# Kernel tuning notes

Measured on AMD Instinct MI355X. Metric: run time of the kernel, lower is better.

Reference implementation:

```python
import jax, jax.numpy as jnp
import numpy as np

N = 32768       # nodes
E = 65536       # directed edges
B = 512         # graphs (N // B = 64 atoms each)
DIM = 64
NUM_FEAT = 14
EDGE_DIM = 4
NET_HID = 128
CONV_STEPS = 12
S2S_STEPS = 3
NSTEM = 1024
NUM_OUT_STEM = 105

leaky = lambda v: jax.nn.leaky_relu(v, 0.01)


def setup_inputs():
    key = jax.random.key(0)
    ks = jax.random.split(key, 30)
    p = lambda i, shape, s=0.1: jax.random.normal(ks[i], shape, jnp.float32) * s
    return {
        'x': jax.random.normal(ks[0], (N, NUM_FEAT), jnp.float32),
        'edge_attr': jax.random.uniform(ks[1], (E, EDGE_DIM), jnp.float32),
        'edge_index': jax.random.randint(ks[2], (2, E), 0, N),
        'batch': jnp.arange(N, dtype=jnp.int32) // (N // B),  # sorted graph ids, all graphs non-empty
        'stem_idx': jax.random.randint(ks[3], (NSTEM,), 0, N),
        'lin0_w': p(4, (DIM, NUM_FEAT)), 'lin0_b': p(5, (DIM,)),
        'net_w1': p(6, (NET_HID, EDGE_DIM)), 'net_b1': p(7, (NET_HID,)),
        'net_w2': p(8, (DIM * DIM, NET_HID), 0.05), 'net_b2': p(9, (DIM * DIM,), 0.05),
        'conv_root': p(10, (DIM, DIM)), 'conv_bias': p(11, (DIM,)),
        'gru_w_ih': p(12, (3 * DIM, DIM)), 'gru_w_hh': p(13, (3 * DIM, DIM)),
        'gru_b_ih': p(14, (3 * DIM,)), 'gru_b_hh': p(15, (3 * DIM,)),
        'lin1_w': p(16, (8 * DIM, DIM)), 'lin1_b': p(17, (8 * DIM,)),
        'lin2_w': p(18, (NUM_OUT_STEM, 8 * DIM)), 'lin2_b': p(19, (NUM_OUT_STEM,)),
        's2s_w_ih': p(20, (4 * DIM, 2 * DIM)), 's2s_w_hh': p(21, (4 * DIM, DIM)),
        's2s_b_ih': p(22, (4 * DIM,)), 's2s_b_hh': p(23, (4 * DIM,)),
        'lin3_w': p(24, (1, 2 * DIM)), 'lin3_b': p(25, (1,)),
    }


def reference(x, edge_attr, edge_index, batch, stem_idx,
              lin0_w, lin0_b, net_w1, net_b1, net_w2, net_b2,
              conv_root, conv_bias, gru_w_ih, gru_w_hh, gru_b_ih, gru_b_hh,
              lin1_w, lin1_b, lin2_w, lin2_b,
              s2s_w_ih, s2s_w_hh, s2s_b_ih, s2s_b_hh, lin3_w, lin3_b):
    src, dst = edge_index[0], edge_index[1]

    out = leaky(x @ lin0_w.T + lin0_b)               # [N, DIM]
    h = out

    # edge-conditioned weights: constant across conv steps (edge_attr fixed), hoist
    W = (leaky(edge_attr @ net_w1.T + net_b1) @ net_w2.T + net_b2).reshape(E, DIM, DIM)

    deg = jax.ops.segment_sum(jnp.ones((E,), jnp.float32), dst, num_segments=N)
    inv_deg = (1.0 / jnp.maximum(deg, 1.0))[:, None]

    def step(carry, _):
        out, h = carry
        # NNConv: gather src feats, per-edge matmul, scatter-mean to dst, plus root term
        msg = jnp.einsum('ei,eio->eo', out[src], W)                           # [E, DIM]
        agg = jax.ops.segment_sum(msg, dst, num_segments=N) * inv_deg        # scatter-mean
        m = leaky(agg + out @ conv_root + conv_bias)
        # GRU cell (torch gate order r, z, n)
        gi = m @ gru_w_ih.T + gru_b_ih
        gh = h @ gru_w_hh.T + gru_b_hh
        ir, iz, i_n = jnp.split(gi, 3, axis=-1)
        hr, hz, hn = jnp.split(gh, 3, axis=-1)
        r = jax.nn.sigmoid(ir + hr)
        z = jax.nn.sigmoid(iz + hz)
        n = jnp.tanh(i_n + r * hn)
        h_new = (1.0 - z) * n + z * h
        return (h_new, h_new), None

    (out, h), _ = jax.lax.scan(step, (out, h), None, length=CONV_STEPS)

    # per-stem head (stem_idx = precomputed flat node indices)
    stem_feat = out[stem_idx]                                                # [NSTEM, DIM]
    per_stem_out = leaky(stem_feat @ lin1_w.T + lin1_b) @ lin2_w.T + lin2_b  # [NSTEM, 105]

    # Set2Set readout (LSTM with torch gate order i, f, g, o)
    q_star = jnp.zeros((B, 2 * DIM), jnp.float32)
    hh = jnp.zeros((B, DIM), jnp.float32)
    cc = jnp.zeros((B, DIM), jnp.float32)
    for _ in range(S2S_STEPS):
        gates = q_star @ s2s_w_ih.T + s2s_b_ih + hh @ s2s_w_hh.T + s2s_b_hh
        gi_, gf_, gg_, go_ = jnp.split(gates, 4, axis=-1)
        cc = jax.nn.sigmoid(gf_) * cc + jax.nn.sigmoid(gi_) * jnp.tanh(gg_)
        hh = jax.nn.sigmoid(go_) * jnp.tanh(cc)
        q = hh                                                               # [B, DIM]
        e = jnp.sum(out * q[batch], axis=-1)                                 # [N]
        emax = jax.ops.segment_max(e, batch, num_segments=B)
        ee = jnp.exp(e - emax[batch])
        a = ee / jax.ops.segment_sum(ee, batch, num_segments=B)[batch]       # segment softmax
        r_read = jax.ops.segment_sum(a[:, None] * out, batch, num_segments=B)
        q_star = jnp.concatenate([q, r_read], axis=-1)

    sout = q_star @ lin3_w.T + lin3_b                                        # [B, 1]
    return sout, per_stem_out


if __name__ == '__main__':
    o = reference(**setup_inputs())
    print(o[0].shape, o[1].shape)
```

## Files before the change

### kernel.cpp

```cpp
#include <hip/hip_runtime.h>
#include <hip/hip_bf16.h>

#define N_NODES   32768
#define N_EDGES   65536
#define NGRAPH    512
#define DIM       64
#define NFEAT     14
#define NHID      128
#define WCOLS     4096
#define NSTEM     1024
#define NOUT      105

typedef __attribute__((ext_vector_type(8))) short short8;
typedef __attribute__((ext_vector_type(4))) float f32x4;

__device__ __forceinline__ float bf2f(unsigned int u16) {
  union { unsigned int i; float f; } c; c.i = u16 << 16; return c.f;
}
__device__ __forceinline__ unsigned short f2bf(float f) {
  union { float f; unsigned int i; } c; c.f = f;
  return (unsigned short)((c.i + 0x7fffu + ((c.i >> 16) & 1u)) >> 16);
}
__device__ __forceinline__ float leaky(float x) { return x > 0.f ? x : 0.01f * x; }
__device__ __forceinline__ float sigm(float x) { return 1.f / (1.f + expf(-x)); }

constexpr size_t ALN(size_t x) { return (x + 255) & ~(size_t)255; }

constexpr size_t OFF_HIDP = 0;
constexpr size_t SZ_HIDP  = (size_t)N_EDGES * NHID * 2;
constexpr size_t OFF_T2T  = ALN(OFF_HIDP + SZ_HIDP);
constexpr size_t SZ_T2T   = (size_t)WCOLS * NHID * 2;
constexpr size_t OFF_B2T  = ALN(OFF_T2T + SZ_T2T);
constexpr size_t SZ_B2T   = (size_t)WCOLS * 4;
constexpr size_t OFF_STATE= ALN(OFF_B2T + SZ_B2T);
constexpr size_t SZ_STATE = (size_t)N_NODES * DIM * 4;
constexpr size_t OFF_AGG  = ALN(OFF_STATE + SZ_STATE);
constexpr size_t SZ_AGG   = SZ_STATE;
constexpr size_t OFF_IDEG = ALN(OFF_AGG + SZ_AGG);
constexpr size_t SZ_IDEG  = (size_t)N_NODES * 4;
constexpr size_t OFF_CNT  = ALN(OFF_IDEG + SZ_IDEG);
constexpr size_t SZ_CNT   = (size_t)N_NODES * 4;
constexpr size_t OFF_RP   = ALN(OFF_CNT + SZ_CNT);
constexpr size_t SZ_RP    = (size_t)(N_NODES + 1) * 4;
constexpr size_t OFF_CUR  = ALN(OFF_RP + SZ_RP);
constexpr size_t SZ_CUR   = (size_t)N_NODES * 4;
constexpr size_t OFF_SRCP = ALN(OFF_CUR + SZ_CUR);
constexpr size_t SZ_SRCP  = (size_t)N_EDGES * 4;
constexpr size_t OFF_DSTP = ALN(OFF_SRCP + SZ_SRCP);
constexpr size_t SZ_DSTP  = (size_t)N_EDGES * 4;
constexpr size_t OFF_EPOS = ALN(OFF_DSTP + SZ_DSTP);
constexpr size_t SZ_EPOS  = (size_t)N_EDGES * 4;
constexpr size_t OFF_BW1  = ALN(OFF_EPOS + SZ_EPOS);
constexpr size_t SZ_BW1   = 256 * 64 * 2;
constexpr size_t OFF_BW2  = ALN(OFF_BW1 + SZ_BW1);
constexpr size_t SZ_BW2   = 192 * 64 * 2;
constexpr size_t OFF_WIH  = ALN(OFF_BW2 + SZ_BW2);
constexpr size_t SZ_WIH   = 128 * 256 * 4;
constexpr size_t OFF_WHH  = ALN(OFF_WIH + SZ_WIH);
constexpr size_t SZ_WHH   = 64 * 256 * 4;
constexpr size_t OFF_SCL  = ALN(OFF_WHH + SZ_WHH);
constexpr size_t SZ_SCL   = (size_t)N_EDGES * 64 * 4;
constexpr size_t OFF_WT   = ALN(OFF_SCL + SZ_SCL);

__global__ void k_deg(const int* __restrict__ dst, int* __restrict__ cnt) {
  int e = blockIdx.x * 256 + threadIdx.x;
  atomicAdd(&cnt[dst[e]], 1);
}
__global__ __launch_bounds__(1024) void k_scan(const int* __restrict__ cnt,
                                               int* __restrict__ rp,
                                               int* __restrict__ cur,
                                               float* __restrict__ ideg) {
  __shared__ int part[1024];
  const int t = threadIdx.x, base = t * 32;
  int s = 0;
  for (int i = 0; i < 32; ++i) s += cnt[base + i];
  part[t] = s;
  __syncthreads();
  for (int off = 1; off < 1024; off <<= 1) {
    int v = (t >= off) ? part[t - off] : 0;
    __syncthreads();
    part[t] += v;
    __syncthreads();
  }
  int run = part[t] - s;
  for (int i = 0; i < 32; ++i) {
    int c = cnt[base + i];
    rp[base + i] = run; cur[base + i] = run;
    ideg[base + i] = 1.0f / fmaxf((float)c, 1.0f);
    run += c;
  }
  if (t == 1023) rp[N_NODES] = run;
}
__global__ void k_permute(const int* __restrict__ src, const int* __restrict__ dst,
                          int* __restrict__ cur, int* __restrict__ src_p,
                          int* __restrict__ dst_p, int* __restrict__ epos) {
  int e = blockIdx.x * 256 + threadIdx.x;
  int d = dst[e];
  int p = atomicAdd(&cur[d], 1);
  src_p[p] = src[e]; dst_p[p] = d; epos[e] = p;
}
__global__ void k_prep_t2(const float* __restrict__ w2, const float* __restrict__ b2,
                          unsigned short* __restrict__ T2t, float* __restrict__ b2t) {
  int gid = blockIdx.x * 256 + threadIdx.x;
  int r = gid >> 7, h = gid & 127;
  int srow = (r & 63) * 64 + (r >> 6);
  T2t[gid] = f2bf(w2[(size_t)srow * 128 + h]);
  if (h == 0) b2t[r] = b2[srow];
}
__global__ void k_prep_gru(const float* __restrict__ root, const float* __restrict__ whh,
                           const float* __restrict__ wih,
                           unsigned short* __restrict__ BW1, unsigned short* __restrict__ BW2) {
  int gid = blockIdx.x * 256 + threadIdx.x;
  if (gid >= 64 * 448) return;
  int i = gid / 448, c = gid % 448;
  if (c < 64)        BW1[c * 64 + i] = f2bf(root[i * 64 + c]);
  else if (c < 256)  BW1[c * 64 + i] = f2bf(whh[(c - 64) * 64 + i]);
  else               BW2[(c - 256) * 64 + i] = f2bf(wih[(c - 256) * 64 + i]);
}
__global__ void k_prep_s2s(const float* __restrict__ wih, const float* __restrict__ whh,
                           float* __restrict__ wihT, float* __restrict__ whhT) {
  int gid = blockIdx.x * 256 + threadIdx.x;
  if (gid < 32768) { int j = gid >> 8, k = gid & 255; wihT[gid] = wih[k * 128 + j]; }
  else { int g2 = gid - 32768; int j = g2 >> 8, k = g2 & 255; whhT[g2] = whh[k * 64 + j]; }
}
__global__ void k_lin0(const float* __restrict__ x, const float* __restrict__ w,
                       const float* __restrict__ b, float* __restrict__ state) {
  int gid = blockIdx.x * 256 + threadIdx.x;
  int n = gid >> 6, o = gid & 63;
  float acc = b[o];
  #pragma unroll
  for (int f = 0; f < NFEAT; ++f) acc += x[(size_t)n * NFEAT + f] * w[o * NFEAT + f];
  state[gid] = leaky(acc);
}
__global__ void k_hidden(const float* __restrict__ ea, const float* __restrict__ w1,
                         const float* __restrict__ b1, const int* __restrict__ epos,
                         unsigned short* __restrict__ hid_p) {
  int gid = blockIdx.x * 256 + threadIdx.x;
  int e = gid >> 7, h = gid & 127;
  float acc = b1[h];
  #pragma unroll
  for (int d = 0; d < 4; ++d) acc += ea[(size_t)e * 4 + d] * w1[h * 4 + d];
  hid_p[(size_t)epos[e] * 128 + h] = f2bf(leaky(acc));
}

#define WG_PAD 136
__global__ __launch_bounds__(256) void k_wgemm(const unsigned short* __restrict__ A,
                                               const unsigned short* __restrict__ Bt,
                                               const float* __restrict__ b2t,
                                               unsigned short* __restrict__ WtP,
                                               unsigned char* __restrict__ W8,
                                               float* __restrict__ SCL,
                                               int peb) {
  __shared__ __align__(16) unsigned short As[64 * WG_PAD];
  __shared__ __align__(16) unsigned short Bs[64 * WG_PAD];
  __shared__ __align__(16) char pk[64][64];
  const int nb = blockIdx.x, mb = blockIdx.y, t = threadIdx.x;
  #pragma unroll
  for (int j = 0; j < 4; ++j) {
    int c = t + 256 * j;
    int row = c >> 4, col8 = (c & 15) * 8;
    *reinterpret_cast<uint4*>(&As[row * WG_PAD + col8]) =
        *reinterpret_cast<const uint4*>(A + (size_t)(mb * 64 + row) * 128 + col8);
    *reinterpret_cast<uint4*>(&Bs[row * WG_PAD + col8]) =
        *reinterpret_cast<const uint4*>(Bt + (size_t)(nb * 64 + row) * 128 + col8);
  }
  __syncthreads();
  const int wv = t >> 6, ln = t & 63, r = ln & 15, g = ln >> 4;
  f32x4 acc[4] = {};
  #pragma unroll
  for (int ks = 0; ks < 4; ++ks) {
    int k0 = ks * 32 + g * 8;
    short8 a = *reinterpret_cast<const short8*>(&As[(wv * 16 + r) * WG_PAD + k0]);
    #pragma unroll
    for (int nt = 0; nt < 4; ++nt) {
      short8 b = *reinterpret_cast<const short8*>(&Bs[(nt * 16 + r) * WG_PAD + k0]);
      acc[nt] = __builtin_amdgcn_mfma_f32_16x16x32_bf16(a, b, acc[nt], 0, 0, 0);
    }
  }
  float bias[4];
  #pragma unroll
  for (int nt = 0; nt < 4; ++nt) bias[nt] = b2t[nb * 64 + nt * 16 + r];

  if (mb * 64 < peb) {
    #pragma unroll
    for (int nt = 0; nt < 4; ++nt) {
      int col = nb * 64 + nt * 16 + r;
      #pragma unroll
      for (int j = 0; j < 4; ++j) {
        int row = mb * 64 + wv * 16 + g * 4 + j;
        WtP[(size_t)row * WCOLS + col] = f2bf(acc[nt][j] + bias[nt]);
      }
    }
  } else {
    #pragma unroll
    for (int j = 0; j < 4; ++j) {
      int e_l = wv * 16 + g * 4 + j;
      float w[4], m = 0.f;
      #pragma unroll
      for (int nt = 0; nt < 4; ++nt) { w[nt] = acc[nt][j] + bias[nt]; m = fmaxf(m, fabsf(w[nt])); }
      m = fmaxf(m, __shfl_xor(m, 1)); m = fmaxf(m, __shfl_xor(m, 2));
      m = fmaxf(m, __shfl_xor(m, 4)); m = fmaxf(m, __shfl_xor(m, 8));
      float inv = m > 0.f ? 127.f / m : 0.f;
      #pragma unroll
      for (int nt = 0; nt < 4; ++nt)
        pk[e_l][nt * 16 + r] = (char)(int)rintf(w[nt] * inv);
      if (r == 0) {
        size_t e8 = (size_t)(mb * 64 - peb) + e_l;
        SCL[e8 * 64 + nb] = m * (1.f / 127.f);
      }
    }
    __syncthreads();
    int e_l = t >> 2, q4 = t & 3;
    size_t e8 = (size_t)(mb * 64 - peb) + e_l;
    *reinterpret_cast<uint4*>(W8 + e8 * 4096 + nb * 64 + q4 * 16) =
        *reinterpret_cast<const uint4*>(&pk[e_l][q4 * 16]);
  }
}

__global__ __launch_bounds__(256) void k_msg_csr(const unsigned short* __restrict__ WtP,
                                                 const unsigned char* __restrict__ W8,
                                                 const float* __restrict__ SCL,
                                                 int peb, int lim8,
                                                 const int* __restrict__ rp,
                                                 const int* __restrict__ src_p,
                                                 const float* __restrict__ state,
                                                 const float* __restrict__ ideg,
                                                 float* __restrict__ agg) {
  const int wv = threadIdx.x >> 6, ln = threadIdx.x & 63;
  const int d = blockIdx.x * 4 + wv;
  const int k0 = rp[d], k1 = rp[d + 1];
  float acc = 0.f;
  for (int k = k0; k < k1; ++k) {
    if (k >= lim8) continue;
    const int src = src_p[k];
    const float sval = state[(size_t)src * 64 + ln];
    if (k < peb) {
      const unsigned short* wp = WtP + (size_t)k * WCOLS + ln * 64;
      #pragma unroll
      for (int j = 0; j < 8; ++j) {
        uint4 v = *reinterpret_cast<const uint4*>(wp + j * 8);
        unsigned int u[4] = {v.x, v.y, v.z, v.w};
        #pragma unroll
        for (int q = 0; q < 4; ++q) {
          float w0 = bf2f(u[q] & 0xffffu);
          union { unsigned int i; float f; } hi; hi.i = u[q] & 0xffff0000u;
          acc = fmaf(__shfl(sval, j * 8 + q * 2), w0, acc);
          acc = fmaf(__shfl(sval, j * 8 + q * 2 + 1), hi.f, acc);
        }
      }
    } else {
      const uint4* wp = reinterpret_cast<const uint4*>(W8 + ((size_t)(k - peb) * 64 + ln) * 64);
      float sub = 0.f;
      #pragma unroll
      for (int j = 0; j < 4; ++j) {
        uint4 v = wp[j];
        unsigned int u[4] = {v.x, v.y, v.z, v.w};
        #pragma unroll
        for (int q = 0; q < 4; ++q) {
          int i0 = j * 16 + q * 4;
          sub = fmaf((float)(int)(char)(u[q] & 0xff),         __shfl(sval, i0),     sub);
          sub = fmaf((float)(int)(char)((u[q] >> 8) & 0xff),  __shfl(sval, i0 + 1), sub);
          sub = fmaf((float)(int)(char)((u[q] >> 16) & 0xff), __shfl(sval, i0 + 2), sub);
          sub = fmaf((float)(int)(char)(u[q] >> 24),          __shfl(sval, i0 + 3), sub);
        }
      }
      acc = fmaf(sub, SCL[(size_t)(k - peb) * 64 + ln], acc);
    }
  }
  agg[(size_t)d * 64 + ln] = acc * ideg[d];
}

#define WM_PAD 136
__global__ __launch_bounds__(256) void k_wmsg(const unsigned short* __restrict__ hid,
                                              const unsigned short* __restrict__ T2t,
                                              const float* __restrict__ b2t,
                                              const float* __restrict__ state,
                                              const int* __restrict__ srcs,
                                              const int* __restrict__ dsts,
                                              const float* __restrict__ ideg,
                                              int e0,
                                              float* __restrict__ agg) {
  __shared__ __align__(16) unsigned short As[64 * WM_PAD];
  __shared__ __align__(16) unsigned short Bs[2][64 * WM_PAD];
  __shared__ __align__(16) float Ss[64][68];
  __shared__ int dstl[64]; __shared__ float idgl[64];
  __shared__ int srcl[64];
  const int t = threadIdx.x;
  const int eb = blockIdx.x * 64;
  if (t < 64) {
    int e = e0 + eb + t;
    srcl[t] = srcs[e];
    int d = dsts[e]; dstl[t] = d; idgl[t] = ideg[d];
  }
  __syncthreads();
  #pragma unroll
  for (int j = 0; j < 4; ++j) {
    int c = t + 256 * j;
    int row = c >> 4, col8 = (c & 15) * 8;
    *reinterpret_cast<uint4*>(&As[row * WM_PAD + col8]) =
        *reinterpret_cast<const uint4*>(hid + (size_t)(eb + row) * 128 + col8);
  }
  #pragma unroll
  for (int j = 0; j < 4; ++j) {
    int c = t + 256 * j;
    int row = c >> 4, q = (c & 15) * 4;
    *reinterpret_cast<float4*>(&Ss[row][q]) =
        *reinterpret_cast<const float4*>(state + (size_t)srcl[row] * 64 + q);
  }
  #pragma unroll
  for (int j = 0; j < 4; ++j) {
    int c = t + 256 * j;
    int row = c >> 4, col8 = (c & 15) * 8;
    *reinterpret_cast<uint4*>(&Bs[0][row * WM_PAD + col8]) =
        *reinterpret_cast<const uint4*>(T2t + (size_t)row * 128 + col8);
  }
  __syncthreads();
  const int wv = t >> 6, ln = t & 63, r = ln & 15, g = ln >> 4;
  for (int nb = 0; nb < 64; ++nb) {
    const int cur = nb & 1;
    if (nb + 1 < 64) {
      #pragma unroll
      for (int j = 0; j < 4; ++j) {
        int c = t + 256 * j;
        int row = c >> 4, col8 = (c & 15) * 8;
        *reinterpret_cast<uint4*>(&Bs[cur ^ 1][row * WM_PAD + col8]) =
            *reinterpret_cast<const uint4*>(T2t + (size_t)((nb + 1) * 64 + row) * 128 + col8);
      }
    }
    f32x4 acc[4] = {};
    #pragma unroll
    for (int ks = 0; ks < 4; ++ks) {
      int k0 = ks * 32 + g * 8;
      short8 a = *reinterpret_cast<const short8*>(&As[(wv * 16 + r) * WM_PAD + k0]);
      #pragma unroll
      for (int nt = 0; nt < 4; ++nt) {
        short8 b = *reinterpret_cast<const short8*>(&Bs[cur][(nt * 16 + r) * WM_PAD + k0]);
        acc[nt] = __builtin_amdgcn_mfma_f32_16x16x32_bf16(a, b, acc[nt], 0, 0, 0);
      }
    }
    float bias[4];
    #pragma unroll
    for (int nt = 0; nt < 4; ++nt) bias[nt] = b2t[nb * 64 + nt * 16 + r];
    float pj[4];
    #pragma unroll
    for (int j = 0; j < 4; ++j) {
      int row = wv * 16 + g * 4 + j;
      float p = 0.f;
      #pragma unroll
      for (int nt = 0; nt < 4; ++nt)
        p += (acc[nt][j] + bias[nt]) * Ss[row][nt * 16 + r];
      pj[j] = p;
    }
    #pragma unroll
    for (int j = 0; j < 4; ++j) {
      float p = pj[j];
      p += __shfl_xor(p, 1); p += __shfl_xor(p, 2);
      p += __shfl_xor(p, 4); p += __shfl_xor(p, 8);
      pj[j] = p;
    }
    if (r == 0) {
      #pragma unroll
      for (int j = 0; j < 4; ++j) {
        int row = wv * 16 + g * 4 + j;
        atomicAdd(&agg[(size_t)dstl[row] * 64 + nb], pj[j] * idgl[row]);
      }
    }
    __syncthreads();
  }
}

#define KPAD 72
__global__ __launch_bounds__(512, 1) void k_gru(const float* __restrict__ agg,
                                                float* __restrict__ state,
                                                const unsigned short* __restrict__ BW1,
                                                const unsigned short* __restrict__ BW2,
                                                const float* __restrict__ conv_bias,
                                                const float* __restrict__ b_ih,
                                                const float* __restrict__ b_hh) {
  __shared__ __align__(16) unsigned short As[128 * KPAD];
  __shared__ __align__(16) unsigned short Ms[128 * KPAD];
  __shared__ __align__(16) unsigned short B1s[256 * KPAD];
  __shared__ __align__(16) unsigned short B2s[192 * KPAD];
  const int t = threadIdx.x;
  const int rowbase = blockIdx.x * 128;
  #pragma unroll
  for (int j = 0; j < 2; ++j) {
    int c = t + 512 * j;
    int row = c >> 3, col8 = (c & 7) * 8;
    const float* sp = state + (size_t)(rowbase + row) * 64 + col8;
    float4 f0 = *reinterpret_cast<const float4*>(sp);
    float4 f1 = *reinterpret_cast<const float4*>(sp + 4);
    short8 hv;
    hv[0] = (short)f2bf(f0.x); hv[1] = (short)f2bf(f0.y);
    hv[2] = (short)f2bf(f0.z); hv[3] = (short)f2bf(f0.w);
    hv[4] = (short)f2bf(f1.x); hv[5] = (short)f2bf(f1.y);
    hv[6] = (short)f2bf(f1.z); hv[7] = (short)f2bf(f1.w);
    *reinterpret_cast<short8*>(&As[row * KPAD + col8]) = hv;
  }
  #pragma unroll
  for (int j = 0; j < 4; ++j) {
    int c = t + 512 * j;
    int row = c >> 3, col8 = (c & 7) * 8;
    *reinterpret_cast<uint4*>(&B1s[row * KPAD + col8]) =
        *reinterpret_cast<const uint4*>(BW1 + row * 64 + col8);
  }
  #pragma unroll
  for (int j = 0; j < 3; ++j) {
    int c = t + 512 * j;
    int row = c >> 3, col8 = (c & 7) * 8;
    *reinterpret_cast<uint4*>(&B2s[row * KPAD + col8]) =
        *reinterpret_cast<const uint4*>(BW2 + row * 64 + col8);
  }
  __syncthreads();
  const int wv = t >> 6, ln = t & 63, r = ln & 15, g = ln >> 4;
  f32x4 acc1[16] = {};
  #pragma unroll
  for (int ks = 0; ks < 2; ++ks) {
    int k0 = ks * 32 + g * 8;
    short8 a = *reinterpret_cast<const short8*>(&As[(wv * 16 + r) * KPAD + k0]);
    #pragma unroll
    for (int nt = 0; nt < 16; ++nt) {
      short8 b = *reinterpret_cast<const short8*>(&B1s[(nt * 16 + r) * KPAD + k0]);
      acc1[nt] = __builtin_amdgcn_mfma_f32_16x16x32_bf16(a, b, acc1[nt], 0, 0, 0);
    }
  }
  #pragma unroll
  for (int nt = 0; nt < 4; ++nt) {
    int col = nt * 16 + r;
    float cb = conv_bias[col];
    #pragma unroll
    for (int j = 0; j < 4; ++j) {
      int lrow = wv * 16 + g * 4 + j;
      float mv = agg[(size_t)(rowbase + lrow) * 64 + col] + acc1[nt][j] + cb;
      Ms[lrow * KPAD + col] = f2bf(leaky(mv));
    }
  }
  __syncthreads();
  f32x4 acc2[12] = {};
  #pragma unroll
  for (int ks = 0; ks < 2; ++ks) {
    int k0 = ks * 32 + g * 8;
    short8 a = *reinterpret_cast<const short8*>(&Ms[(wv * 16 + r) * KPAD + k0]);
    #pragma unroll
    for (int nt = 0; nt < 12; ++nt) {
      short8 b = *reinterpret_cast<const short8*>(&B2s[(nt * 16 + r) * KPAD + k0]);
      acc2[nt] = __builtin_amdgcn_mfma_f32_16x16x32_bf16(a, b, acc2[nt], 0, 0, 0);
    }
  }
  #pragma unroll
  for (int nt = 0; nt < 4; ++nt) {
    int o = nt * 16 + r;
    float bir = b_ih[o],       bhr = b_hh[o];
    float biz = b_ih[64 + o],  bhz = b_hh[64 + o];
    float bin = b_ih[128 + o], bhn = b_hh[128 + o];
    #pragma unroll
    for (int j = 0; j < 4; ++j) {
      size_t gidx = (size_t)(rowbase + wv * 16 + g * 4 + j) * 64 + o;
      float rr = sigm(acc2[nt][j] + bir + acc1[4 + nt][j] + bhr);
      float zz = sigm(acc2[4 + nt][j] + biz + acc1[8 + nt][j] + bhz);
      float nn = tanhf(acc2[8 + nt][j] + bin + rr * (acc1[12 + nt][j] + bhn));
      float hold = state[gidx];
      state[gidx] = (1.f - zz) * nn + zz * hold;
    }
  }
}

__global__ __launch_bounds__(256) void k_s2s(const float* __restrict__ state,
                                             const float* __restrict__ wihT,
                                             const float* __restrict__ whhT,
                                             const float* __restrict__ b_ih,
                                             const float* __restrict__ b_hh,
                                             const float* __restrict__ lin3_w,
                                             const float* __restrict__ lin3_b,
                                             float* __restrict__ d_out) {
  __shared__ float tile[64 * 65];
  __shared__ float qs[128], hhs[64], ccs[64], gates[256], attw[64];
  const int g = blockIdx.x, t = threadIdx.x;
  for (int c = t; c < 64 * 64; c += 256) {
    int row = c >> 6, col = c & 63;
    tile[row * 65 + col] = state[(size_t)(g * 64 + row) * 64 + col];
  }
  if (t < 128) qs[t] = 0.f;
  if (t < 64) { hhs[t] = 0.f; ccs[t] = 0.f; }
  __syncthreads();
  for (int it = 0; it < 3; ++it) {
    float acc = b_ih[t] + b_hh[t];
    for (int j = 0; j < 128; ++j) acc += qs[j] * wihT[j * 256 + t];
    for (int j = 0; j < 64; ++j)  acc += hhs[j] * whhT[j * 256 + t];
    gates[t] = acc;
    __syncthreads();
    if (t < 64) {
      float ci = sigm(gates[t]), cf = sigm(gates[64 + t]);
      float cg = tanhf(gates[128 + t]), co = sigm(gates[192 + t]);
      float c2 = cf * ccs[t] + ci * cg;
      ccs[t] = c2;
      float h2 = co * tanhf(c2);
      hhs[t] = h2; qs[t] = h2;
    }
    __syncthreads();
    if (t < 64) {
      float e = 0.f;
      for (int o = 0; o < 64; ++o) e += tile[t * 65 + o] * qs[o];
      float m = e;
      for (int off = 32; off; off >>= 1) m = fmaxf(m, __shfl_xor(m, off));
      float ex = expf(e - m);
      float s = ex;
      for (int off = 32; off; off >>= 1) s += __shfl_xor(s, off);
      attw[t] = ex / s;
    }
    __syncthreads();
    if (t < 64) {
      float racc = 0.f;
      for (int j = 0; j < 64; ++j) racc += attw[j] * tile[j * 65 + t];
      qs[64 + t] = racc;
    }
    __syncthreads();
  }
  if (t < 64) {
    float v = qs[t] * lin3_w[t] + qs[64 + t] * lin3_w[64 + t];
    for (int off = 32; off; off >>= 1) v += __shfl_xor(v, off);
    if (t == 0) d_out[g] = v + lin3_b[0];
  }
}

__global__ __launch_bounds__(512) void k_stem(const float* __restrict__ state,
                                              const int* __restrict__ stem_idx,
                                              const float* __restrict__ w1,
                                              const float* __restrict__ b1,
                                              const float* __restrict__ w2,
                                              const float* __restrict__ b2,
                                              float* __restrict__ d_out) {
  __shared__ float feat[64];
  __shared__ float hidl[512];
  const int t = threadIdx.x, s = blockIdx.x;
  if (t < 64) feat[t] = state[(size_t)stem_idx[s] * 64 + t];
  __syncthreads();
  {
    const float* wr = w1 + (size_t)t * 64;
    float a0 = 0.f, a1 = 0.f, a2 = 0.f, a3 = 0.f;
    #pragma unroll
    for (int i = 0; i < 64; i += 16) {
      float4 x0 = *reinterpret_cast<const float4*>(wr + i);
      float4 x1 = *reinterpret_cast<const float4*>(wr + i + 4);
      float4 x2 = *reinterpret_cast<const float4*>(wr + i + 8);
      float4 x3 = *reinterpret_cast<const float4*>(wr + i + 12);
      a0 += x0.x*feat[i]    + x0.y*feat[i+1]  + x0.z*feat[i+2]  + x0.w*feat[i+3];
      a1 += x1.x*feat[i+4]  + x1.y*feat[i+5]  + x1.z*feat[i+6]  + x1.w*feat[i+7];
      a2 += x2.x*feat[i+8]  + x2.y*feat[i+9]  + x2.z*feat[i+10] + x2.w*feat[i+11];
      a3 += x3.x*feat[i+12] + x3.y*feat[i+13] + x3.z*feat[i+14] + x3.w*feat[i+15];
    }
    hidl[t] = leaky(a0 + a1 + a2 + a3 + b1[t]);
  }
  __syncthreads();
  if (t < 4 * NOUT) {
    int o = t >> 2, q = t & 3;
    const float* wr = w2 + (size_t)o * 512 + q * 128;
    const float* hr = hidl + q * 128;
    float a0 = 0.f, a1 = 0.f, a2 = 0.f, a3 = 0.f;
    #pragma unroll
    for (int k = 0; k < 128; k += 16) {
      float4 x0 = *reinterpret_cast<const float4*>(wr + k);
      float4 x1 = *reinterpret_cast<const float4*>(wr + k + 4);
      float4 x2 = *reinterpret_cast<const float4*>(wr + k + 8);
      float4 x3 = *reinterpret_cast<const float4*>(wr + k + 12);
      a0 += x0.x*hr[k]    + x0.y*hr[k+1]  + x0.z*hr[k+2]  + x0.w*hr[k+3];
      a1 += x1.x*hr[k+4]  + x1.y*hr[k+5]  + x1.z*hr[k+6]  + x1.w*hr[k+7];
      a2 += x2.x*hr[k+8]  + x2.y*hr[k+9]  + x2.z*hr[k+10] + x2.w*hr[k+11];
      a3 += x3.x*hr[k+12] + x3.y*hr[k+13] + x3.z*hr[k+14] + x3.w*hr[k+15];
    }
    float p = a0 + a1 + a2 + a3;
    p += __shfl_xor(p, 1); p += __shfl_xor(p, 2);
    if (q == 0) d_out[512 + (size_t)s * NOUT + o] = p + b2[o];
  }
}

extern "C" void kernel_launch(void* const* d_in, const int* in_sizes, int n_in,
                              void* d_out, int out_size, void* d_ws, size_t ws_size,
                              hipStream_t stream) {
  (void)in_sizes; (void)n_in; (void)out_size;
  if (ws_size < OFF_WT) return;

  const long avail = (long)(ws_size - OFF_WT);
  long peb = (avail - (long)N_EDGES * 4096) / 4096;
  if (peb < 0) peb = 0;
  if (peb > N_EDGES) peb = N_EDGES;
  peb &= ~63L;
  long pe8 = 0, te = 0;
  if (peb >= N_EDGES) { peb = N_EDGES; }
  else {
    long rem = (avail - peb * 8192) / 4096;
    pe8 = N_EDGES - peb < rem ? N_EDGES - peb : rem;
    if (pe8 < 0) pe8 = 0;
    pe8 &= ~63L;
    te = N_EDGES - peb - pe8;
  }
  const int PEb = (int)peb, LIM8 = (int)(peb + pe8), TE = (int)te;

  const float* x         = (const float*)d_in[0];
  const float* edge_attr = (const float*)d_in[1];
  const int*   eidx      = (const int*)d_in[2];
  const int*   stem_idx  = (const int*)d_in[4];
  const float* lin0_w = (const float*)d_in[5];
  const float* lin0_b = (const float*)d_in[6];
  const float* net_w1 = (const float*)d_in[7];
  const float* net_b1 = (const float*)d_in[8];
  const float* net_w2 = (const float*)d_in[9];
  const float* net_b2 = (const float*)d_in[10];
  const float* conv_root = (const float*)d_in[11];
  const float* conv_bias = (const float*)d_in[12];
  const float* gru_w_ih = (const float*)d_in[13];
  const float* gru_w_hh = (const float*)d_in[14];
  const float* gru_b_ih = (const float*)d_in[15];
  const float* gru_b_hh = (const float*)d_in[16];
  const float* lin1_w = (const float*)d_in[17];
  const float* lin1_b = (const float*)d_in[18];
  const float* lin2_w = (const float*)d_in[19];
  const float* lin2_b = (const float*)d_in[20];
  const float* s2s_w_ih = (const float*)d_in[21];
  const float* s2s_w_hh = (const float*)d_in[22];
  const float* s2s_b_ih = (const float*)d_in[23];
  const float* s2s_b_hh = (const float*)d_in[24];
  const float* lin3_w = (const float*)d_in[25];
  const float* lin3_b = (const float*)d_in[26];

  char* ws = (char*)d_ws;
  unsigned short* hid_p = (unsigned short*)(ws + OFF_HIDP);
  unsigned short* T2t  = (unsigned short*)(ws + OFF_T2T);
  float*          b2t  = (float*)(ws + OFF_B2T);
  float*          state= (float*)(ws + OFF_STATE);
  float*          agg  = (float*)(ws + OFF_AGG);
  float*          ideg = (float*)(ws + OFF_IDEG);
  int*            cnt  = (int*)(ws + OFF_CNT);
  int*            rp   = (int*)(ws + OFF_RP);
  int*            cur  = (int*)(ws + OFF_CUR);
  int*            src_p= (int*)(ws + OFF_SRCP);
  int*            dst_p= (int*)(ws + OFF_DSTP);
  int*            epos = (int*)(ws + OFF_EPOS);
  unsigned short* BW1  = (unsigned short*)(ws + OFF_BW1);
  unsigned short* BW2  = (unsigned short*)(ws + OFF_BW2);
  float*          wihT = (float*)(ws + OFF_WIH);
  float*          whhT = (float*)(ws + OFF_WHH);
  float*          SCL  = (float*)(ws + OFF_SCL);
  unsigned short* WtP  = (unsigned short*)(ws + OFF_WT);
  unsigned char*  W8   = (unsigned char*)(ws + OFF_WT + (size_t)PEb * 8192);
  float* out = (float*)d_out;

  const int* src = eidx;
  const int* dst = eidx + N_EDGES;

  hipMemsetAsync(cnt, 0, SZ_CNT, stream);
  k_deg<<<N_EDGES / 256, 256, 0, stream>>>(dst, cnt);
  k_scan<<<1, 1024, 0, stream>>>(cnt, rp, cur, ideg);
  k_permute<<<N_EDGES / 256, 256, 0, stream>>>(src, dst, cur, src_p, dst_p, epos);
  k_prep_t2<<<(WCOLS * NHID) / 256, 256, 0, stream>>>(net_w2, net_b2, T2t, b2t);
  k_prep_gru<<<112, 256, 0, stream>>>(conv_root, gru_w_hh, gru_w_ih, BW1, BW2);
  k_prep_s2s<<<192, 256, 0, stream>>>(s2s_w_ih, s2s_w_hh, wihT, whhT);
  k_lin0<<<(N_NODES * DIM) / 256, 256, 0, stream>>>(x, lin0_w, lin0_b, state);
  k_hidden<<<(N_EDGES * NHID) / 256, 256, 0, stream>>>(edge_attr, net_w1, net_b1,
                                                       epos, hid_p);
  if (LIM8 > 0)
    k_wgemm<<<dim3(WCOLS / 64, LIM8 / 64), 256, 0, stream>>>(hid_p, T2t, b2t,
                                                             WtP, W8, SCL, PEb);

  for (int s = 0; s < 12; ++s) {
    k_msg_csr<<<N_NODES / 4, 256, 0, stream>>>(WtP, W8, SCL, PEb, LIM8,
                                               rp, src_p, state, ideg, agg);
    if (TE > 0)
      k_wmsg<<<TE / 64, 256, 0, stream>>>(hid_p + (size_t)LIM8 * NHID, T2t, b2t,
                                          state, src_p, dst_p, ideg, LIM8, agg);
    k_gru<<<N_NODES / 128, 512, 0, stream>>>(agg, state, BW1, BW2, conv_bias,
                                             gru_b_ih, gru_b_hh);
  }

  k_s2s<<<NGRAPH, 256, 0, stream>>>(state, wihT, whhT, s2s_b_ih, s2s_b_hh,
                                    lin3_w, lin3_b, out);
  k_stem<<<NSTEM, 512, 0, stream>>>(state, stem_idx, lin1_w, lin1_b,
                                    lin2_w, lin2_b, out);
}
```

Before: 2.069 ms.

## Store all precomputed edge weights as int8 with a coalesced interleaved layout

```diff
diff --git a/kernel.cpp b/kernel.cpp
--- a/kernel.cpp
+++ b/kernel.cpp
@@ -147,10 +147,8 @@
 __global__ __launch_bounds__(256) void k_wgemm(const unsigned short* __restrict__ A,
                                                const unsigned short* __restrict__ Bt,
                                                const float* __restrict__ b2t,
-                                               unsigned short* __restrict__ WtP,
                                                unsigned char* __restrict__ W8,
-                                               float* __restrict__ SCL,
-                                               int peb) {
+                                               float* __restrict__ SCL) {
   __shared__ __align__(16) unsigned short As[64 * WG_PAD];
   __shared__ __align__(16) unsigned short Bs[64 * WG_PAD];
   __shared__ __align__(16) char pk[64][64];
@@ -180,47 +178,35 @@
   float bias[4];
   #pragma unroll
   for (int nt = 0; nt < 4; ++nt) bias[nt] = b2t[nb * 64 + nt * 16 + r];
-
-  if (mb * 64 < peb) {
-    #pragma unroll
-    for (int nt = 0; nt < 4; ++nt) {
-      int col = nb * 64 + nt * 16 + r;
-      #pragma unroll
-      for (int j = 0; j < 4; ++j) {
-        int row = mb * 64 + wv * 16 + g * 4 + j;
-        WtP[(size_t)row * WCOLS + col] = f2bf(acc[nt][j] + bias[nt]);
-      }
-    }
-  } else {
-    #pragma unroll
-    for (int j = 0; j < 4; ++j) {
-      int e_l = wv * 16 + g * 4 + j;
-      float w[4], m = 0.f;
-      #pragma unroll
-      for (int nt = 0; nt < 4; ++nt) { w[nt] = acc[nt][j] + bias[nt]; m = fmaxf(m, fabsf(w[nt])); }
-      m = fmaxf(m, __shfl_xor(m, 1)); m = fmaxf(m, __shfl_xor(m, 2));
-      m = fmaxf(m, __shfl_xor(m, 4)); m = fmaxf(m, __shfl_xor(m, 8));
-      float inv = m > 0.f ? 127.f / m : 0.f;
-      #pragma unroll
-      for (int nt = 0; nt < 4; ++nt)
-        pk[e_l][nt * 16 + r] = (char)(int)rintf(w[nt] * inv);
-      if (r == 0) {
-        size_t e8 = (size_t)(mb * 64 - peb) + e_l;
-        SCL[e8 * 64 + nb] = m * (1.f / 127.f);
-      }
-    }
-    __syncthreads();
-    int e_l = t >> 2, q4 = t & 3;
-    size_t e8 = (size_t)(mb * 64 - peb) + e_l;
-    *reinterpret_cast<uint4*>(W8 + e8 * 4096 + nb * 64 + q4 * 16) =
-        *reinterpret_cast<const uint4*>(&pk[e_l][q4 * 16]);
-  }
-}
-
-__global__ __launch_bounds__(256) void k_msg_csr(const unsigned short* __restrict__ WtP,
-                                                 const unsigned char* __restrict__ W8,
+  #pragma unroll
+  for (int j = 0; j < 4; ++j) {
+    int e_l = wv * 16 + g * 4 + j;
+    float w[4], m = 0.f;
+    #pragma unroll
+    for (int nt = 0; nt < 4; ++nt) { w[nt] = acc[nt][j] + bias[nt]; m = fmaxf(m, fabsf(w[nt])); }
+    m = fmaxf(m, __shfl_xor(m, 1)); m = fmaxf(m, __shfl_xor(m, 2));
+    m = fmaxf(m, __shfl_xor(m, 4)); m = fmaxf(m, __shfl_xor(m, 8));
+    float inv = m > 0.f ? 127.f / m : 0.f;
+    #pragma unroll
+    for (int nt = 0; nt < 4; ++nt)
+      pk[e_l][nt * 16 + r] = (char)(int)rintf(w[nt] * inv);
+    if (r == 0) {
+      size_t e8 = (size_t)mb * 64 + e_l;
+      SCL[e8 * 64 + nb] = m * (1.f / 127.f);
+    }
+  }
+  __syncthreads();
+  {
+    int e_l = t >> 2, jc = t & 3;
+    size_t e8 = (size_t)mb * 64 + e_l;
+    *reinterpret_cast<uint4*>(W8 + e8 * 4096 + jc * 1024 + nb * 16) =
+        *reinterpret_cast<const uint4*>(&pk[e_l][jc * 16]);
+  }
+}
+
+__global__ __launch_bounds__(256) void k_msg_csr(const unsigned char* __restrict__ W8,
                                                  const float* __restrict__ SCL,
-                                                 int peb, int lim8,
+                                                 int lim8,
                                                  const int* __restrict__ rp,
                                                  const int* __restrict__ src_p,
                                                  const float* __restrict__ state,
@@ -234,38 +220,22 @@
     if (k >= lim8) continue;
     const int src = src_p[k];
     const float sval = state[(size_t)src * 64 + ln];
-    if (k < peb) {
-      const unsigned short* wp = WtP + (size_t)k * WCOLS + ln * 64;
+    const unsigned char* wp = W8 + (size_t)k * 4096 + ln * 16;
+    float sub = 0.f;
+    #pragma unroll
+    for (int j = 0; j < 4; ++j) {
+      uint4 v = *reinterpret_cast<const uint4*>(wp + j * 1024);
+      unsigned int u[4] = {v.x, v.y, v.z, v.w};
       #pragma unroll
-      for (int j = 0; j < 8; ++j) {
-        uint4 v = *reinterpret_cast<const uint4*>(wp + j * 8);
-        unsigned int u[4] = {v.x, v.y, v.z, v.w};
-        #pragma unroll
-        for (int q = 0; q < 4; ++q) {
-          float w0 = bf2f(u[q] & 0xffffu);
-          union { unsigned int i; float f; } hi; hi.i = u[q] & 0xffff0000u;
-          acc = fmaf(__shfl(sval, j * 8 + q * 2), w0, acc);
-          acc = fmaf(__shfl(sval, j * 8 + q * 2 + 1), hi.f, acc);
-        }
+      for (int q = 0; q < 4; ++q) {
+        int i0 = j * 16 + q * 4;
+        sub = fmaf((float)(int)(char)(u[q] & 0xff),         __shfl(sval, i0),     sub);
+        sub = fmaf((float)(int)(char)((u[q] >> 8) & 0xff),  __shfl(sval, i0 + 1), sub);
+        sub = fmaf((float)(int)(char)((u[q] >> 16) & 0xff), __shfl(sval, i0 + 2), sub);
+        sub = fmaf((float)(int)(char)(u[q] >> 24),          __shfl(sval, i0 + 3), sub);
       }
-    } else {
-      const uint4* wp = reinterpret_cast<const uint4*>(W8 + ((size_t)(k - peb) * 64 + ln) * 64);
-      float sub = 0.f;
-      #pragma unroll
-      for (int j = 0; j < 4; ++j) {
-        uint4 v = wp[j];
-        unsigned int u[4] = {v.x, v.y, v.z, v.w};
-        #pragma unroll
-        for (int q = 0; q < 4; ++q) {
-          int i0 = j * 16 + q * 4;
-          sub = fmaf((float)(int)(char)(u[q] & 0xff),         __shfl(sval, i0),     sub);
-          sub = fmaf((float)(int)(char)((u[q] >> 8) & 0xff),  __shfl(sval, i0 + 1), sub);
-          sub = fmaf((float)(int)(char)((u[q] >> 16) & 0xff), __shfl(sval, i0 + 2), sub);
-          sub = fmaf((float)(int)(char)(u[q] >> 24),          __shfl(sval, i0 + 3), sub);
-        }
-      }
-      acc = fmaf(sub, SCL[(size_t)(k - peb) * 64 + ln], acc);
-    }
+    }
+    acc = fmaf(sub, SCL[(size_t)k * 64 + ln], acc);
   }
   agg[(size_t)d * 64 + ln] = acc * ideg[d];
 }
@@ -580,21 +550,11 @@
   (void)in_sizes; (void)n_in; (void)out_size;
   if (ws_size < OFF_WT) return;
 
-  const long avail = (long)(ws_size - OFF_WT);
-  long peb = (avail - (long)N_EDGES * 4096) / 4096;
-  if (peb < 0) peb = 0;
-  if (peb > N_EDGES) peb = N_EDGES;
-  peb &= ~63L;
-  long pe8 = 0, te = 0;
-  if (peb >= N_EDGES) { peb = N_EDGES; }
-  else {
-    long rem = (avail - peb * 8192) / 4096;
-    pe8 = N_EDGES - peb < rem ? N_EDGES - peb : rem;
-    if (pe8 < 0) pe8 = 0;
-    pe8 &= ~63L;
-    te = N_EDGES - peb - pe8;
-  }
-  const int PEb = (int)peb, LIM8 = (int)(peb + pe8), TE = (int)te;
+  long pe8 = (long)((ws_size - OFF_WT) / 4096);
+  if (pe8 > N_EDGES) pe8 = N_EDGES;
+  pe8 &= ~63L;
+  const int LIM8 = (int)pe8;
+  const int TE = N_EDGES - LIM8;
 
   const float* x         = (const float*)d_in[0];
   const float* edge_attr = (const float*)d_in[1];
@@ -641,8 +601,7 @@
   float*          wihT = (float*)(ws + OFF_WIH);
   float*          whhT = (float*)(ws + OFF_WHH);
   float*          SCL  = (float*)(ws + OFF_SCL);
-  unsigned short* WtP  = (unsigned short*)(ws + OFF_WT);
-  unsigned char*  W8   = (unsigned char*)(ws + OFF_WT + (size_t)PEb * 8192);
+  unsigned char*  W8   = (unsigned char*)(ws + OFF_WT);
   float* out = (float*)d_out;
 
   const int* src = eidx;
@@ -659,15 +618,14 @@
   k_hidden<<<(N_EDGES * NHID) / 256, 256, 0, stream>>>(edge_attr, net_w1, net_b1,
                                                        epos, hid_p);
   if (LIM8 > 0)
-    k_wgemm<<<dim3(WCOLS / 64, LIM8 / 64), 256, 0, stream>>>(hid_p, T2t, b2t,
-                                                             WtP, W8, SCL, PEb);
+    k_wgemm<<<dim3(WCOLS / 64, LIM8 / 64), 256, 0, stream>>>(hid_p, T2t, b2t, W8, SCL);
 
   for (int s = 0; s < 12; ++s) {
-    k_msg_csr<<<N_NODES / 4, 256, 0, stream>>>(WtP, W8, SCL, PEb, LIM8,
-                                               rp, src_p, state, ideg, agg);
+    k_msg_csr<<<N_NODES / 4, 256, 0, stream>>>(W8, SCL, LIM8, rp, src_p,
+                                               state, ideg, agg);
     if (TE > 0)
-      k_wmsg<<<TE / 64, 256, 0, stream>>>(hid_p + (size_t)LIM8 * NHID, T2t, b2t,
-                                          state, src_p, dst_p, ideg, LIM8, agg);
+      k_wmsg<<<(TE + 63) / 64, 256, 0, stream>>>(hid_p + (size_t)LIM8 * NHID, T2t, b2t,
+                                                 state, src_p, dst_p, ideg, LIM8, agg);
     k_gru<<<N_NODES / 128, 512, 0, stream>>>(agg, state, BW1, BW2, conv_bias,
                                              gru_b_ih, gru_b_hh);
   }
```

Result: no change. 2.090 ms (+1.0%).
